# Kernel optimization log

Measured on AMD Instinct MI355X. Metric: run time of the kernel, lower is better.

The kernel has to match this reference:

```python
import jax, jax.numpy as jnp
import numpy as np

NEG_SLOPE = 0.2  # DGL GATConv default leaky_relu slope


def gat_conv(x, src, dst, W, attn_l, attn_r, bias, res_W):
    """DGL GATConv (eval mode, residual=True with linear res_fc, bias).
    x: [N, F_in]; src/dst: [E]; W: [F_in, H*D]; attn_l/r: [H, D];
    bias: [H*D]; res_W: [F_in, H*D]. Returns [N, H, D]."""
    N = x.shape[0]
    H, D = attn_l.shape
    feat = (x @ W).reshape(N, H, D)
    el = jnp.sum(feat * attn_l, axis=-1)  # [N, H]
    er = jnp.sum(feat * attn_r, axis=-1)  # [N, H]
    e = jax.nn.leaky_relu(el[src] + er[dst], NEG_SLOPE)  # [E, H]
    # edge softmax over incoming edges of each dst node (numerically stable)
    m = jnp.full((N, H), -jnp.inf, dtype=e.dtype).at[dst].max(e)
    ex = jnp.exp(e - m[dst])
    s = jnp.zeros((N, H), dtype=e.dtype).at[dst].add(ex)
    alpha = ex / s[dst]  # [E, H]
    # scatter-aggregate messages alpha * feat[src] into dst
    rst = jnp.zeros((N, H, D), dtype=x.dtype).at[dst].add(alpha[:, :, None] * feat[src])
    rst = rst + (x @ res_W).reshape(N, H, D) + bias.reshape(1, H, D)
    return rst


def setup_inputs() -> dict:
    key = jax.random.key(0)
    N, E, F_IN, HID, OUT, H = 20000, 320000, 128, 128, 128, 4
    ks = jax.random.split(key, 32)
    ki = iter(range(32))

    def rn(shape, scale=0.05):
        return jax.random.normal(ks[next(ki)], shape, dtype=jnp.float32) * scale

    inp = {
        "n_feat": jax.random.normal(ks[next(ki)], (N, F_IN), dtype=jnp.float32),
        "src": jax.random.randint(ks[next(ki)], (E,), 0, N, dtype=jnp.int32),
        "dst": jax.random.randint(ks[next(ki)], (E,), 0, N, dtype=jnp.int32),
        # input GATConv: F_IN -> H x HID
        "W0": rn((F_IN, H * HID)), "al0": rn((H, HID)), "ar0": rn((H, HID)),
        "b0": rn((H * HID,)), "rW0": rn((F_IN, H * HID)),
        "DW0": rn((H * HID, HID)), "Db0": rn((HID,)),
        # middle GATConv: HID -> H x HID
        "W1": rn((HID, H * HID)), "al1": rn((H, HID)), "ar1": rn((H, HID)),
        "b1": rn((H * HID,)), "rW1": rn((HID, H * HID)),
        "DW1": rn((H * HID, HID)), "Db1": rn((HID,)),
        # output GATConv: HID -> H x OUT
        "W2": rn((HID, H * OUT)), "al2": rn((H, OUT)), "ar2": rn((H, OUT)),
        "b2": rn((H * OUT,)), "rW2": rn((HID, H * OUT)),
    }
    return inp


def reference(n_feat, src, dst,
              W0, al0, ar0, b0, rW0, DW0, Db0,
              W1, al1, ar1, b1, rW1, DW1, Db1,
              W2, al2, ar2, b2, rW2):
    N = n_feat.shape[0]
    relu = jax.nn.relu
    # input GAT block
    h = relu(gat_conv(n_feat, src, dst, W0, al0, ar0, b0, rW0))  # [N, H, HID]
    h = relu(h.reshape(N, -1) @ DW0 + Db0)                        # [N, HID]
    # middle GAT block
    h = relu(gat_conv(h, src, dst, W1, al1, ar1, b1, rW1))
    h = relu(h.reshape(N, -1) @ DW1 + Db1)
    # output GAT + head-mean + graph max pooling (single graph)
    h = relu(gat_conv(h, src, dst, W2, al2, ar2, b2, rW2))        # [N, H, OUT]
    h = relu(jnp.mean(h, axis=-2))                                 # [N, OUT]
    return jnp.max(h, axis=0, keepdims=True)                       # [1, OUT]
```

## Files before the change

### kernel.cpp

```cpp
#include <hip/hip_runtime.h>
#include <hip/hip_bf16.h>


typedef __attribute__((ext_vector_type(8))) short bf16x8;
typedef __attribute__((ext_vector_type(4))) float f32x4;
typedef __hip_bfloat16 bf16_t;

__device__ __forceinline__ unsigned int pack_bf16(float lo, float hi) {
  return (((unsigned int)__bfloat16_as_ushort(__float2bfloat16(hi))) << 16) |
         (unsigned int)__bfloat16_as_ushort(__float2bfloat16(lo));
}

__device__ __forceinline__ void gload_lds16(const void* g, void* l) {
  __builtin_amdgcn_global_load_lds(
      (const __attribute__((address_space(1))) void*)g,
      (__attribute__((address_space(3))) void*)l, 16, 0, 0);
}

__global__ __launch_bounds__(256) void mega_prep(
    const float* __restrict__ W0, const float* __restrict__ rW0,
    const float* __restrict__ W1, const float* __restrict__ rW1,
    const float* __restrict__ W2, const float* __restrict__ rW2,
    const float* __restrict__ DW0, const float* __restrict__ DW1,
    const float* __restrict__ al0, const float* __restrict__ ar0,
    const float* __restrict__ al1, const float* __restrict__ ar1,
    const float* __restrict__ al2, const float* __restrict__ ar2,
    const float* __restrict__ n_feat, bf16_t* __restrict__ wts,
    float* __restrict__ ALR, bf16_t* __restrict__ xbf,
    int* __restrict__ counts, float* __restrict__ d_out_f, int N) {
  __shared__ float tile[32][33];
  int b = blockIdx.x, tid = threadIdx.x;
  int r = tid >> 5, c = tid & 31;

  if (b < 384) {
    int mat = b >> 6;
    int t = b & 63;
    int kt = t >> 4, nt = t & 15;
    int L = mat >> 1, isR = mat & 1;
    const float* S = (L == 0) ? (isR ? rW0 : W0)
                   : (L == 1) ? (isR ? rW1 : W1) : (isR ? rW2 : W2);
    bf16_t* D = wts + L * 131072 + isR * 65536;
#pragma unroll
    for (int rr = 0; rr < 4; rr++)
      tile[r + rr * 8][c] = S[(kt * 32 + r + rr * 8) * 512 + nt * 32 + c];
    __syncthreads();
#pragma unroll
    for (int rr = 0; rr < 4; rr++)
      D[(nt * 32 + r + rr * 8) * 128 + kt * 32 + c] =
          __float2bfloat16(tile[c][r + rr * 8]);
  } else if (b < 512) {
    int i = b - 384;
    int mat = i >> 6;
    int t = i & 63;
    int kt = t & 15, nt = t >> 4;
    const float* S = mat ? DW1 : DW0;
    bf16_t* D = wts + 393216 + mat * 65536;
#pragma unroll
    for (int rr = 0; rr < 4; rr++)
      tile[r + rr * 8][c] = S[(kt * 32 + r + rr * 8) * 128 + nt * 32 + c];
    __syncthreads();
#pragma unroll
    for (int rr = 0; rr < 4; rr++)
      D[(nt * 32 + r + rr * 8) * 512 + kt * 32 + c] =
          __float2bfloat16(tile[c][r + rr * 8]);
  } else if (b < 524) {
    int idx = (b - 512) * 256 + tid;
    if (idx < 3072) {
      int L = idx >> 10;
      int k = (idx >> 3) & 127;
      int cc = idx & 7;
      int h = cc & 3;
      const float* W = (L == 0) ? W0 : (L == 1) ? W1 : W2;
      const float* a = (cc < 4) ? ((L == 0) ? al0 : (L == 1) ? al1 : al2)
                                : ((L == 0) ? ar0 : (L == 1) ? ar1 : ar2);
      float s = 0.f;
      for (int d = 0; d < 128; d++) s += W[k * 512 + h * 128 + d] * a[h * 128 + d];
      ALR[idx] = s;
    }
  } else if (b < 3024) {
    int i = ((b - 524) * 256 + tid) * 4;
    if (i < N * 128) {
      float4 v = *(const float4*)(n_feat + i);
      xbf[i + 0] = __float2bfloat16(v.x);
      xbf[i + 1] = __float2bfloat16(v.y);
      xbf[i + 2] = __float2bfloat16(v.z);
      xbf[i + 3] = __float2bfloat16(v.w);
    }
  } else {
    for (int i = tid; i < N; i += 256) counts[i] = 0;
    if (tid < 128) d_out_f[tid] = 0.f;
  }
}

__global__ __launch_bounds__(256) void gemm128el(
    const bf16_t* __restrict__ A, const bf16_t* __restrict__ Bt,
    const float* __restrict__ ALRl, bf16_t* __restrict__ C,
    float* __restrict__ el, float* __restrict__ er, int M, int ldc, int K) {
  __shared__ bf16_t As[128 * 64];
  __shared__ bf16_t Bs[128 * 64];
  int tid = threadIdx.x;
  int rowBase = blockIdx.y * 128;

  if (blockIdx.x == 8) {
    float* sALR = (float*)As;
#pragma unroll
    for (int j = 0; j < 4; j++) sALR[tid * 4 + j] = ALRl[tid * 4 + j];
    __syncthreads();
    int row = rowBase + (tid >> 1);
    int half = tid & 1;
    if (row < M) {
      const bf16_t* xr = A + (size_t)row * K + half * 64;
      float s[8] = {};
#pragma unroll
      for (int g = 0; g < 8; g++) {
        bf16x8 v = *(const bf16x8*)(xr + g * 8);
#pragma unroll
        for (int e = 0; e < 8; e++) {
          float f = __uint_as_float(((unsigned int)(unsigned short)v[e]) << 16);
          const float* Ak = sALR + (half * 64 + g * 8 + e) * 8;
#pragma unroll
          for (int cc = 0; cc < 8; cc++) s[cc] += f * Ak[cc];
        }
      }
#pragma unroll
      for (int cc = 0; cc < 8; cc++) s[cc] += __shfl_xor(s[cc], 1);
      if (half == 0)
        *(float4*)(el + row * 4) = make_float4(s[0], s[1], s[2], s[3]);
      else
        *(float4*)(er + row * 4) = make_float4(s[4], s[5], s[6], s[7]);
    }
    return;
  }

  int lane = tid & 63, wave = tid >> 6;
  int q = lane >> 4, r16 = lane & 15;
  int wm = (wave >> 1) * 64, wn = (wave & 1) * 64;
  int colBase = blockIdx.x * 128;

  f32x4 acc[4][4] = {};

  for (int k0 = 0; k0 < K; k0 += 64) {
#pragma unroll
    for (int p = 0; p < 4; p++) {
      int slotb = (wave * 4 + p) * 64;
      int s = slotb + lane;
      int r = s >> 3;
      int c = (s & 7) ^ (r & 7);
      int gr = rowBase + r;
      if (gr > M - 1) gr = M - 1;
      gload_lds16(A + (size_t)gr * K + k0 + c * 8, (char*)As + (size_t)slotb * 16);
      gload_lds16(Bt + (size_t)(colBase + r) * K + k0 + c * 8,
                  (char*)Bs + (size_t)slotb * 16);
    }
    __syncthreads();
#pragma unroll
    for (int ks = 0; ks < 64; ks += 32) {
      int koff = ks >> 3;
      bf16x8 af[4], bfr[4];
#pragma unroll
      for (int i = 0; i < 4; i++) {
        int R = wm + i * 16 + r16;
        int slot = R * 8 + ((q + koff) ^ (R & 7));
        af[i] = *(const bf16x8*)((const char*)As + (size_t)slot * 16);
      }
#pragma unroll
      for (int j = 0; j < 4; j++) {
        int R = wn + j * 16 + r16;
        int slot = R * 8 + ((q + koff) ^ (R & 7));
        bfr[j] = *(const bf16x8*)((const char*)Bs + (size_t)slot * 16);
      }
#pragma unroll
      for (int i = 0; i < 4; i++)
#pragma unroll
        for (int j = 0; j < 4; j++)
          acc[i][j] = __builtin_amdgcn_mfma_f32_16x16x32_bf16(af[i], bfr[j], acc[i][j], 0, 0, 0);
    }
    __syncthreads();
  }

  int odd = lane & 1;
  int colb0 = r16 & ~1;
#pragma unroll
  for (int i = 0; i < 4; i++) {
#pragma unroll
    for (int r = 0; r < 4; r++) {
      int row = rowBase + wm + i * 16 + q * 4 + r;
#pragma unroll
      for (int jp = 0; jp < 2; jp++) {
        float a0 = acc[i][2 * jp][r];
        float a1 = acc[i][2 * jp + 1][r];
        float p0 = __shfl_xor(a0, 1);
        float p1 = __shfl_xor(a1, 1);
        float lo = odd ? p1 : a0;
        float hi = odd ? a1 : p0;
        int col = colBase + wn + (2 * jp + odd) * 16 + colb0;
        if (row < M)
          *(unsigned int*)(C + (size_t)row * ldc + col) = pack_bf16(lo, hi);
      }
    }
  }
}

__global__ __launch_bounds__(256) void mfma_gemm64(
    const bf16_t* __restrict__ A, const bf16_t* __restrict__ Bt,
    const float* __restrict__ bias, bf16_t* __restrict__ C,
    int M, int ldc, int K) {
  __shared__ bf16_t As[64 * 64];
  __shared__ bf16_t Bs[64 * 64];
  int tid = threadIdx.x;
  int lane = tid & 63, wave = tid >> 6;
  int q = lane >> 4, r16 = lane & 15;
  int wm = (wave >> 1) * 32, wn = (wave & 1) * 32;
  int rowBase = blockIdx.y * 64, colBase = blockIdx.x * 64;

  f32x4 acc[2][2] = {};

  for (int k0 = 0; k0 < K; k0 += 64) {
#pragma unroll
    for (int p = 0; p < 2; p++) {
      int slotb = (wave * 2 + p) * 64;
      int s = slotb + lane;
      int r = s >> 3;
      int c = (s & 7) ^ (r & 7);
      int gr = rowBase + r;
      if (gr > M - 1) gr = M - 1;
      gload_lds16(A + (size_t)gr * K + k0 + c * 8, (char*)As + (size_t)slotb * 16);
      gload_lds16(Bt + (size_t)(colBase + r) * K + k0 + c * 8,
                  (char*)Bs + (size_t)slotb * 16);
    }
    __syncthreads();
#pragma unroll
    for (int ks = 0; ks < 64; ks += 32) {
      int koff = ks >> 3;
      bf16x8 af[2], bfr[2];
#pragma unroll
      for (int i = 0; i < 2; i++) {
        int R = wm + i * 16 + r16;
        int slot = R * 8 + ((q + koff) ^ (R & 7));
        af[i] = *(const bf16x8*)((const char*)As + (size_t)slot * 16);
      }
#pragma unroll
      for (int j = 0; j < 2; j++) {
        int R = wn + j * 16 + r16;
        int slot = R * 8 + ((q + koff) ^ (R & 7));
        bfr[j] = *(const bf16x8*)((const char*)Bs + (size_t)slot * 16);
      }
#pragma unroll
      for (int i = 0; i < 2; i++)
#pragma unroll
        for (int j = 0; j < 2; j++)
          acc[i][j] = __builtin_amdgcn_mfma_f32_16x16x32_bf16(af[i], bfr[j], acc[i][j], 0, 0, 0);
    }
    __syncthreads();
  }

  int odd = lane & 1;
  int colb0 = r16 & ~1;
#pragma unroll
  for (int i = 0; i < 2; i++) {
#pragma unroll
    for (int r = 0; r < 4; r++) {
      int row = rowBase + wm + i * 16 + q * 4 + r;
      float a0 = acc[i][0][r];
      float a1 = acc[i][1][r];
      float p0 = __shfl_xor(a0, 1);
      float p1 = __shfl_xor(a1, 1);
      float lo = odd ? p1 : a0;
      float hi = odd ? a1 : p0;
      int col = colBase + wn + odd * 16 + colb0;
      if (row < M) {
        float o0 = fmaxf(lo + bias[col], 0.f);
        float o1 = fmaxf(hi + bias[col + 1], 0.f);
        *(unsigned int*)(C + (size_t)row * ldc + col) = pack_bf16(o0, o1);
      }
    }
  }
}

__global__ __launch_bounds__(256) void count_kernel(const int* __restrict__ dst,
                                                    int* __restrict__ counts, int E) {
  int i = blockIdx.x * blockDim.x + threadIdx.x;
  if (i < E) atomicAdd(&counts[dst[i]], 1);
}

__global__ __launch_bounds__(1024) void scan_kernel(const int* __restrict__ counts,
                                                    int* __restrict__ row_ptr,
                                                    int* __restrict__ cursor, int N) {
  __shared__ int sums[1024];
  int t = threadIdx.x;
  int chunk = (N + 1023) / 1024;
  int begin = t * chunk;
  int end = begin + chunk;
  if (end > N) end = N;
  int s = 0;
  for (int i = begin; i < end; i++) s += counts[i];
  sums[t] = s;
  __syncthreads();
  for (int off = 1; off < 1024; off <<= 1) {
    int v = (t >= off) ? sums[t - off] : 0;
    __syncthreads();
    sums[t] += v;
    __syncthreads();
  }
  int run = (t == 0) ? 0 : sums[t - 1];
  for (int i = begin; i < end; i++) {
    row_ptr[i] = run;
    cursor[i] = run;
    run += counts[i];
  }
  if (t == 1023) row_ptr[N] = sums[1023];
}

__global__ __launch_bounds__(256) void scatter_kernel(
    const int* __restrict__ src, const int* __restrict__ dst,
    int* __restrict__ cursor, int* __restrict__ edge_src, int E) {
  int i = blockIdx.x * blockDim.x + threadIdx.x;
  if (i < E) {
    int d = dst[i];
    int pos = atomicAdd(&cursor[d], 1);
    edge_src[pos] = src[i];
  }
}

__global__ __launch_bounds__(256) void gat_agg_kernel(
    const bf16_t* __restrict__ fused,
    const float* __restrict__ el, const float* __restrict__ er,
    const float* __restrict__ bias, const int* __restrict__ row_ptr,
    const int* __restrict__ edge_src, bf16_t* __restrict__ out, int N) {
  __shared__ float accL[4][64][8];
  __shared__ float ssumL[4][4];
  int n = blockIdx.x;
  int tid = threadIdx.x;
  int wave = tid >> 6, lane = tid & 63;
  int hh = lane >> 4;
  int start = row_ptr[n];
  int deg = row_ptr[n + 1] - start;
  float er_h = er[n * 4 + hh];

  float acc[8] = {};
  float ssum = 0.f;
  const bf16_t* fbase = fused + (size_t)lane * 8;
  for (int i = wave; i < deg; i += 4) {
    int s = edge_src[start + i];
    float e = el[s * 4 + hh] + er_h;
    e = (e > 0.f) ? e : 0.2f * e;
    float w = __expf(e);
    ssum += w;
    uint4 f = *(const uint4*)(fbase + (size_t)s * 1024);
    unsigned int u[4] = {f.x, f.y, f.z, f.w};
#pragma unroll
    for (int j = 0; j < 4; j++) {
      acc[2 * j] += w * __uint_as_float(u[j] << 16);
      acc[2 * j + 1] += w * __uint_as_float(u[j] & 0xffff0000u);
    }
  }
  *(float4*)&accL[wave][lane][0] = make_float4(acc[0], acc[1], acc[2], acc[3]);
  *(float4*)&accL[wave][lane][4] = make_float4(acc[4], acc[5], acc[6], acc[7]);
  if ((lane & 15) == 0) ssumL[wave][hh] = ssum;
  __syncthreads();

  int d = tid * 2;
  int l = d >> 3, j = d & 7;
  float a0 = 0.f, a1 = 0.f;
#pragma unroll
  for (int w = 0; w < 4; w++) {
    a0 += accL[w][l][j];
    a1 += accL[w][l][j + 1];
  }
  int h = tid >> 6;
  float ssum4 = ssumL[0][h] + ssumL[1][h] + ssumL[2][h] + ssumL[3][h];
  float inv = (deg > 0) ? 1.f / ssum4 : 0.f;
  unsigned int ru = *(const unsigned int*)(fused + (size_t)n * 1024 + 512 + d);
  float2 bv = *(const float2*)(bias + d);
  float o0 = fmaxf(a0 * inv + __uint_as_float(ru << 16) + bv.x, 0.f);
  float o1 = fmaxf(a1 * inv + __uint_as_float(ru & 0xffff0000u) + bv.y, 0.f);
  *(unsigned int*)(out + (size_t)n * 512 + d) = pack_bf16(o0, o1);
}

__global__ __launch_bounds__(128) void pool_kernel(const bf16_t* __restrict__ g,
                                                   float* __restrict__ out, int N) {
  int d = threadIdx.x;
  float mx = 0.f;
  for (int n = blockIdx.x; n < N; n += gridDim.x) {
    const bf16_t* p = g + (size_t)n * 512 + d;
    float v = 0.25f * (__bfloat162float(p[0]) + __bfloat162float(p[128]) +
                       __bfloat162float(p[256]) + __bfloat162float(p[384]));
    mx = fmaxf(mx, v);
  }
  atomicMax((int*)out + d, __float_as_int(mx));
}

extern "C" void kernel_launch(void* const* d_in, const int* in_sizes, int n_in,
                              void* d_out, int out_size, void* d_ws, size_t ws_size,
                              hipStream_t stream) {
  const float* n_feat = (const float*)d_in[0];
  const int* src = (const int*)d_in[1];
  const int* dst = (const int*)d_in[2];
  const float* W0 = (const float*)d_in[3];
  const float* al0 = (const float*)d_in[4];
  const float* ar0 = (const float*)d_in[5];
  const float* b0 = (const float*)d_in[6];
  const float* rW0 = (const float*)d_in[7];
  const float* DW0 = (const float*)d_in[8];
  const float* Db0 = (const float*)d_in[9];
  const float* W1 = (const float*)d_in[10];
  const float* al1 = (const float*)d_in[11];
  const float* ar1 = (const float*)d_in[12];
  const float* b1 = (const float*)d_in[13];
  const float* rW1 = (const float*)d_in[14];
  const float* DW1 = (const float*)d_in[15];
  const float* Db1 = (const float*)d_in[16];
  const float* W2 = (const float*)d_in[17];
  const float* al2 = (const float*)d_in[18];
  const float* ar2 = (const float*)d_in[19];
  const float* b2 = (const float*)d_in[20];
  const float* rW2 = (const float*)d_in[21];

  const int N = in_sizes[0] / 128;
  const int E = in_sizes[1];

  bf16_t* xbf = (bf16_t*)d_ws;
  bf16_t* fusedFR = xbf + (size_t)N * 128;
  bf16_t* outC = fusedFR + (size_t)N * 1024;
  bf16_t* denseD = outC + (size_t)N * 512;
  bf16_t* wts = denseD + (size_t)N * 128;
  float* ALR = (float*)(wts + 524288);
  float* el = ALR + 3072;
  float* er = el + (size_t)N * 4;
  int* counts = (int*)(er + (size_t)N * 4);
  int* row_ptr = counts + N;
  int* cursor = row_ptr + (N + 1);
  int* edge_src = cursor + N;

  bf16_t* FW0 = wts;
  bf16_t* FW1 = wts + 131072;
  bf16_t* FW2 = wts + 262144;
  bf16_t* DWt0 = wts + 393216;
  bf16_t* DWt1 = wts + 458752;

  mega_prep<<<3025, 256, 0, stream>>>(
      W0, rW0, W1, rW1, W2, rW2, DW0, DW1,
      al0, ar0, al1, ar1, al2, ar2,
      n_feat, wts, ALR, xbf, counts, (float*)d_out, N);

  count_kernel<<<(E + 255) / 256, 256, 0, stream>>>(dst, counts, E);
  scan_kernel<<<1, 1024, 0, stream>>>(counts, row_ptr, cursor, N);
  scatter_kernel<<<(E + 255) / 256, 256, 0, stream>>>(src, dst, cursor, edge_src, E);

  dim3 gF(9, (N + 127) / 128);
  dim3 gD(2, (N + 63) / 64);

  gemm128el<<<gF, 256, 0, stream>>>(xbf, FW0, ALR, fusedFR, el, er, N, 1024, 128);
  gat_agg_kernel<<<N, 256, 0, stream>>>(fusedFR, el, er, b0, row_ptr, edge_src, outC, N);
  mfma_gemm64<<<gD, 256, 0, stream>>>(outC, DWt0, Db0, denseD, N, 128, 512);

  gemm128el<<<gF, 256, 0, stream>>>(denseD, FW1, ALR + 1024, fusedFR, el, er, N, 1024, 128);
  gat_agg_kernel<<<N, 256, 0, stream>>>(fusedFR, el, er, b1, row_ptr, edge_src, outC, N);
  mfma_gemm64<<<gD, 256, 0, stream>>>(outC, DWt1, Db1, denseD, N, 128, 512);

  gemm128el<<<gF, 256, 0, stream>>>(denseD, FW2, ALR + 2048, fusedFR, el, er, N, 1024, 128);
  gat_agg_kernel<<<N, 256, 0, stream>>>(fusedFR, el, er, b2, row_ptr, edge_src, outC, N);

  pool_kernel<<<256, 128, 0, stream>>>(outC, (float*)d_out, N);
}
```

Baseline: 444.9 us.

## Fuse edge counting into first GEMM and pooling into last aggregation

The standalone count kernel is removed and its work moves into extra blocks (blockIdx.x==9) of the first feature GEMM, so degree counting runs alongside the matmul. The final aggregation writes head-mean values straight into 64 striped partial-max slots with atomics instead of storing the bf16 output, and a tiny finish kernel reduces those slots. This saves two launches and a full write and read of the last layer's output, at the cost of extra atomics and one more block synchronisation in the last aggregation.

```diff
diff --git a/kernel.cpp b/kernel.cpp
--- a/kernel.cpp
+++ b/kernel.cpp
@@ -27,7 +27,7 @@
     const float* __restrict__ al2, const float* __restrict__ ar2,
     const float* __restrict__ n_feat, bf16_t* __restrict__ wts,
     float* __restrict__ ALR, bf16_t* __restrict__ xbf,
-    int* __restrict__ counts, float* __restrict__ d_out_f, int N) {
+    int* __restrict__ counts, float* __restrict__ partials, int N) {
   __shared__ float tile[32][33];
   int b = blockIdx.x, tid = threadIdx.x;
   int r = tid >> 5, c = tid & 31;
@@ -88,18 +88,27 @@
     }
   } else {
     for (int i = tid; i < N; i += 256) counts[i] = 0;
-    if (tid < 128) d_out_f[tid] = 0.f;
-  }
-}
-
+    for (int i = tid; i < 64 * 128; i += 256) partials[i] = 0.f;
+  }
+}
+
+template <bool COUNT>
 __global__ __launch_bounds__(256) void gemm128el(
     const bf16_t* __restrict__ A, const bf16_t* __restrict__ Bt,
     const float* __restrict__ ALRl, bf16_t* __restrict__ C,
-    float* __restrict__ el, float* __restrict__ er, int M, int ldc, int K) {
+    float* __restrict__ el, float* __restrict__ er, int M, int ldc, int K,
+    const int* __restrict__ dst, int* __restrict__ counts, int E) {
   __shared__ bf16_t As[128 * 64];
   __shared__ bf16_t Bs[128 * 64];
   int tid = threadIdx.x;
   int rowBase = blockIdx.y * 128;
+
+  if (COUNT && blockIdx.x == 9) {
+    int stride = gridDim.y * 256;
+    for (int i = blockIdx.y * 256 + tid; i < E; i += stride)
+      atomicAdd(&counts[dst[i]], 1);
+    return;
+  }
 
   if (blockIdx.x == 8) {
     float* sALR = (float*)As;
@@ -275,12 +284,6 @@
       }
     }
   }
-}
-
-__global__ __launch_bounds__(256) void count_kernel(const int* __restrict__ dst,
-                                                    int* __restrict__ counts, int E) {
-  int i = blockIdx.x * blockDim.x + threadIdx.x;
-  if (i < E) atomicAdd(&counts[dst[i]], 1);
 }
 
 __global__ __launch_bounds__(1024) void scan_kernel(const int* __restrict__ counts,
@@ -322,11 +325,13 @@
   }
 }
 
+template <bool POOL>
 __global__ __launch_bounds__(256) void gat_agg_kernel(
     const bf16_t* __restrict__ fused,
     const float* __restrict__ el, const float* __restrict__ er,
     const float* __restrict__ bias, const int* __restrict__ row_ptr,
-    const int* __restrict__ edge_src, bf16_t* __restrict__ out, int N) {
+    const int* __restrict__ edge_src, bf16_t* __restrict__ out,
+    float* __restrict__ partials, int N) {
   __shared__ float accL[4][64][8];
   __shared__ float ssumL[4][4];
   int n = blockIdx.x;
@@ -374,20 +379,31 @@
   float2 bv = *(const float2*)(bias + d);
   float o0 = fmaxf(a0 * inv + __uint_as_float(ru << 16) + bv.x, 0.f);
   float o1 = fmaxf(a1 * inv + __uint_as_float(ru & 0xffff0000u) + bv.y, 0.f);
-  *(unsigned int*)(out + (size_t)n * 512 + d) = pack_bf16(o0, o1);
-}
-
-__global__ __launch_bounds__(128) void pool_kernel(const bf16_t* __restrict__ g,
-                                                   float* __restrict__ out, int N) {
+
+  if (!POOL) {
+    *(unsigned int*)(out + (size_t)n * 512 + d) = pack_bf16(o0, o1);
+  } else {
+    float2* red = (float2*)accL;
+    __syncthreads();
+    red[tid] = make_float2(o0, o1);
+    __syncthreads();
+    if (tid < 64) {
+      float m0 = 0.25f * (red[tid].x + red[tid + 64].x + red[tid + 128].x + red[tid + 192].x);
+      float m1 = 0.25f * (red[tid].y + red[tid + 64].y + red[tid + 128].y + red[tid + 192].y);
+      float* slot = partials + (n & 63) * 128;
+      atomicMax((int*)slot + 2 * tid, __float_as_int(m0));
+      atomicMax((int*)slot + 2 * tid + 1, __float_as_int(m1));
+    }
+  }
+}
+
+__global__ __launch_bounds__(128) void pool_finish(const float* __restrict__ partials,
+                                                   float* __restrict__ out) {
   int d = threadIdx.x;
-  float mx = 0.f;
-  for (int n = blockIdx.x; n < N; n += gridDim.x) {
-    const bf16_t* p = g + (size_t)n * 512 + d;
-    float v = 0.25f * (__bfloat162float(p[0]) + __bfloat162float(p[128]) +
-                       __bfloat162float(p[256]) + __bfloat162float(p[384]));
-    mx = fmaxf(mx, v);
-  }
-  atomicMax((int*)out + d, __float_as_int(mx));
+  float m = 0.f;
+#pragma unroll 8
+  for (int s = 0; s < 64; s++) m = fmaxf(m, partials[s * 128 + d]);
+  out[d] = m;
 }
 
 extern "C" void kernel_launch(void* const* d_in, const int* in_sizes, int n_in,
@@ -427,7 +443,8 @@
   float* ALR = (float*)(wts + 524288);
   float* el = ALR + 3072;
   float* er = el + (size_t)N * 4;
-  int* counts = (int*)(er + (size_t)N * 4);
+  float* partials = er + (size_t)N * 4;
+  int* counts = (int*)(partials + 64 * 128);
   int* row_ptr = counts + N;
   int* cursor = row_ptr + (N + 1);
   int* edge_src = cursor + N;
@@ -441,25 +458,29 @@
   mega_prep<<<3025, 256, 0, stream>>>(
       W0, rW0, W1, rW1, W2, rW2, DW0, DW1,
       al0, ar0, al1, ar1, al2, ar2,
-      n_feat, wts, ALR, xbf, counts, (float*)d_out, N);
-
-  count_kernel<<<(E + 255) / 256, 256, 0, stream>>>(dst, counts, E);
+      n_feat, wts, ALR, xbf, counts, partials, N);
+
+  int nRow = (N + 127) / 128;
+  dim3 gF0(10, nRow);
+  dim3 gF(9, nRow);
+  dim3 gD(2, (N + 63) / 64);
+
+  gemm128el<true><<<gF0, 256, 0, stream>>>(xbf, FW0, ALR, fusedFR, el, er,
+                                           N, 1024, 128, dst, counts, E);
   scan_kernel<<<1, 1024, 0, stream>>>(counts, row_ptr, cursor, N);
   scatter_kernel<<<(E + 255) / 256, 256, 0, stream>>>(src, dst, cursor, edge_src, E);
 
-  dim3 gF(9, (N + 127) / 128);
-  dim3 gD(2, (N + 63) / 64);
-
-  gemm128el<<<gF, 256, 0, stream>>>(xbf, FW0, ALR, fusedFR, el, er, N, 1024, 128);
-  gat_agg_kernel<<<N, 256, 0, stream>>>(fusedFR, el, er, b0, row_ptr, edge_src, outC, N);
+  gat_agg_kernel<false><<<N, 256, 0, stream>>>(fusedFR, el, er, b0, row_ptr,
+                                               edge_src, outC, nullptr, N);
   mfma_gemm64<<<gD, 256, 0, stream>>>(outC, DWt0, Db0, denseD, N, 128, 512);
-
-  gemm128el<<<gF, 256, 0, stream>>>(denseD, FW1, ALR + 1024, fusedFR, el, er, N, 1024, 128);
-  gat_agg_kernel<<<N, 256, 0, stream>>>(fusedFR, el, er, b1, row_ptr, edge_src, outC, N);
+  gemm128el<false><<<gF, 256, 0, stream>>>(denseD, FW1, ALR + 1024, fusedFR,
+                                           el, er, N, 1024, 128, nullptr, nullptr, 0);
+  gat_agg_kernel<false><<<N, 256, 0, stream>>>(fusedFR, el, er, b1, row_ptr,
+                                               edge_src, outC, nullptr, N);
   mfma_gemm64<<<gD, 256, 0, stream>>>(outC, DWt1, Db1, denseD, N, 128, 512);
-
-  gemm128el<<<gF, 256, 0, stream>>>(denseD, FW2, ALR + 2048, fusedFR, el, er, N, 1024, 128);
-  gat_agg_kernel<<<N, 256, 0, stream>>>(fusedFR, el, er, b2, row_ptr, edge_src, outC, N);
-
-  pool_kernel<<<256, 128, 0, stream>>>(outC, (float*)d_out, N);
-}
+  gemm128el<false><<<gF, 256, 0, stream>>>(denseD, FW2, ALR + 2048, fusedFR,
+                                           el, er, N, 1024, 128, nullptr, nullptr, 0);
+  gat_agg_kernel<true><<<N, 256, 0, stream>>>(fusedFR, el, er, b2, row_ptr,
+                                              edge_src, nullptr, partials, N);
+  pool_finish<<<1, 128, 0, stream>>>(partials, (float*)d_out);
+}
```

Measured after the change: 413.5 us, median of 2. -7.0%, faster.
